# Kernel optimization log

Measured on AMD Instinct MI355X. Metric: run time of the kernel, lower is better.

## Reference

```python
import jax, jax.numpy as jnp
import numpy as np
jax.config.update('jax_enable_x64', True)

H = 16          # tree height -> n = 2**H
TP = 16         # parallel coordinate dims
F = 2
DIV = 2
K = F * H // DIV          # 16
N = 1 << H                # 65536
EMB = 1_000_000
T = 2048                  # rows in this block


def setup_inputs() -> dict:
    key = jax.random.key(0)
    k1, k2, k3 = jax.random.split(key, 3)
    # location table: signed ints in [1-n, n), as in torch.randint(1-n, n, ...)
    locations = jax.random.randint(k1, (EMB, TP), 1 - N, N, dtype=jnp.int64)
    pos_idx = jax.random.randint(k2, (T,), 0, EMB, dtype=jnp.int64)
    norm = jax.random.uniform(k3, (T, 1, 1), dtype=jnp.float32)
    return {"locations": locations, "pos_idx": pos_idx, "norm": norm}


def _generate_random_masks(key, sz):
    # masks[i] uniform in [0, 2**i) per level i  (note: & binds looser than -,
    # so torch code computes rand & (2**i - 1))
    upper = (jnp.int64(1) << jnp.arange(H, dtype=jnp.int64)) - 1  # (H,)
    rn = jax.random.randint(key, (H, sz, K, TP), 0, N, dtype=jnp.int64)
    masks = rn & upper[:, None, None, None]
    return jnp.transpose(masks, (1, 0, 2, 3))  # (sz, H, K, TP)


def _connection(key, ori_int):
    # ori_int: (T, TP) int64
    kmask, kperm = jax.random.split(key)
    flip_masks = (jnp.int64(1) << jnp.arange(H, dtype=jnp.int64))[None, :, None]  # (1,H,1)
    flipped = ori_int[:, None, :] ^ flip_masks                    # (T, H, TP)
    rmasks = _generate_random_masks(kmask, flipped.shape[0])      # (T, H, K, TP)
    result = (flipped[:, :, None, :] ^ rmasks).reshape(T, H * K, TP)
    loc = jnp.concatenate([result, ori_int[:, None, :], -result], axis=1)  # (T, 2HK+1, TP)
    perm = jax.random.permutation(kperm, loc.shape[1])
    return loc[:, perm, :]


def _distance(coord1, coord2, norm):
    # sign product: +1 if same sign (>=0 vs <0), else -1
    sg = (jnp.where(coord1 >= 0, 1.0, -1.0) * jnp.where(coord2 >= 0, 1.0, -1.0)).astype(jnp.float32)
    xor = jnp.abs(coord1) ^ jnp.abs(coord2)
    _, e = jnp.frexp((xor + 1).astype(jnp.float32))  # frexp exponent == bit length
    s = e.astype(jnp.float32) / H
    return sg * (1.0 - s) * norm


def reference(locations, pos_idx, norm):
    # gather this block's node locations (irregular gather from large table)
    ori = locations[pos_idx]                         # (T, TP)
    key = jax.random.key(42)
    loc = _connection(key, ori)                      # (T, 2HK+1, TP) candidate neighbors
    # distances from each candidate back to the original location
    return _distance(loc, ori[:, None, :], norm)     # (T, 2HK+1, TP) float32
```

## Files before the change

### kernel.cpp

```cpp
#include <hip/hip_runtime.h>
#include <stdint.h>


#define H_   16
#define TP_  16
#define K_   16
#define T_   2048
#define NC   513
#define ROWS 4
#define GRID (T_ / ROWS)

typedef float f32x4 __attribute__((ext_vector_type(4)));

struct TFPair { uint32_t a, b; };

__host__ __device__ constexpr uint32_t rotl32(uint32_t x, int r) {
  return (x << r) | (x >> (32 - r));
}

__host__ __device__ constexpr TFPair tf2x32(uint32_t k0, uint32_t k1,
                                            uint32_t x0, uint32_t x1) {
  uint32_t ks0 = k0, ks1 = k1, ks2 = k0 ^ k1 ^ 0x1BD11BDAu;
  x0 += ks0; x1 += ks1;
  x0 += x1; x1 = rotl32(x1, 13); x1 ^= x0;
  x0 += x1; x1 = rotl32(x1, 15); x1 ^= x0;
  x0 += x1; x1 = rotl32(x1, 26); x1 ^= x0;
  x0 += x1; x1 = rotl32(x1,  6); x1 ^= x0;
  x0 += ks1; x1 += ks2 + 1u;
  x0 += x1; x1 = rotl32(x1, 17); x1 ^= x0;
  x0 += x1; x1 = rotl32(x1, 29); x1 ^= x0;
  x0 += x1; x1 = rotl32(x1, 16); x1 ^= x0;
  x0 += x1; x1 = rotl32(x1, 24); x1 ^= x0;
  x0 += ks2; x1 += ks0 + 2u;
  x0 += x1; x1 = rotl32(x1, 13); x1 ^= x0;
  x0 += x1; x1 = rotl32(x1, 15); x1 ^= x0;
  x0 += x1; x1 = rotl32(x1, 26); x1 ^= x0;
  x0 += x1; x1 = rotl32(x1,  6); x1 ^= x0;
  x0 += ks0; x1 += ks1 + 3u;
  x0 += x1; x1 = rotl32(x1, 17); x1 ^= x0;
  x0 += x1; x1 = rotl32(x1, 29); x1 ^= x0;
  x0 += x1; x1 = rotl32(x1, 16); x1 ^= x0;
  x0 += x1; x1 = rotl32(x1, 24); x1 ^= x0;
  x0 += ks1; x1 += ks2 + 4u;
  x0 += x1; x1 = rotl32(x1, 13); x1 ^= x0;
  x0 += x1; x1 = rotl32(x1, 15); x1 ^= x0;
  x0 += x1; x1 = rotl32(x1, 26); x1 ^= x0;
  x0 += x1; x1 = rotl32(x1,  6); x1 ^= x0;
  x0 += ks2; x1 += ks0 + 5u;
  return {x0, x1};
}

constexpr TFPair KM = tf2x32(0u, 42u, 0u, 0u);
constexpr TFPair KP = tf2x32(0u, 42u, 0u, 1u);
constexpr TFPair C2 = tf2x32(KM.a, KM.b, 0u, 1u);
constexpr uint32_t KLO0 = C2.a, KLO1 = C2.b;
constexpr TFPair SB = tf2x32(KP.a, KP.b, 0u, 1u);
constexpr uint32_t KSUB0 = SB.a, KSUB1 = SB.b;

struct Keys { uint32_t v[NC]; };
constexpr Keys make_keys() {
  Keys k{};
  for (int i = 0; i < NC; ++i) {
    TFPair r = tf2x32(KSUB0, KSUB1, 0u, (uint32_t)i);
    k.v[i] = r.a ^ r.b;
  }
  return k;
}
constexpr Keys KEYS = make_keys();

#define PART_SZ 33
struct Part { int v[PART_SZ]; };
constexpr Part make_part(int lo) {
  Part p{};
  for (int m = lo; m < lo + PART_SZ && m < NC; ++m) {
    uint32_t km = KEYS.v[m];
    int rank = 0;
    for (int j = 0; j < NC; ++j) {
      uint32_t kj = KEYS.v[j];
      if (kj < km || (kj == km && j < m)) ++rank;
    }
    p.v[m - lo] = rank;
  }
  return p;
}
constexpr Part PT0  = make_part(0),   PT1  = make_part(33),
               PT2  = make_part(66),  PT3  = make_part(99),
               PT4  = make_part(132), PT5  = make_part(165),
               PT6  = make_part(198), PT7  = make_part(231),
               PT8  = make_part(264), PT9  = make_part(297),
               PT10 = make_part(330), PT11 = make_part(363),
               PT12 = make_part(396), PT13 = make_part(429),
               PT14 = make_part(462), PT15 = make_part(495);

struct IPerm { int v[NC]; };
constexpr IPerm merge_parts() {
  IPerm r{};
  const Part* ps[16] = {&PT0, &PT1, &PT2,  &PT3,  &PT4,  &PT5,  &PT6,  &PT7,
                        &PT8, &PT9, &PT10, &PT11, &PT12, &PT13, &PT14, &PT15};
  for (int c = 0; c < 16; ++c)
    for (int i = 0; i < PART_SZ; ++i) {
      int m = c * PART_SZ + i;
      if (m < NC) r.v[m] = ps[c]->v[i];
    }
  return r;
}
constexpr IPerm IPERM = merge_parts();
constexpr int C_ORI = IPERM.v[256];

struct CTab { uint32_t v[256]; };
constexpr CTab make_ctab() {
  CTab c{};
  for (int j = 0; j < 256; ++j)
    c.v[j] = (uint32_t)IPERM.v[j] | ((uint32_t)IPERM.v[j + 257] << 16);
  return c;
}
constexpr CTab CTAB = make_ctab();
__device__ __constant__ CTab d_ctab = CTAB;

__global__ __launch_bounds__(256, 4) void dist_kernel(
    const int* __restrict__ locations, const int* __restrict__ pos_idx,
    const float* __restrict__ norm, float* __restrict__ out) {
  __shared__ __align__(16) float buf[NC * TP_];

  const int tid = (int)threadIdx.x;
  const int tp  = tid & 15;
  const int jl  = tid >> 4;
  const int t0  = (int)blockIdx.x * ROWS;

  uint32_t ct[16];
#pragma unroll
  for (int i = 0; i < 16; ++i) ct[i] = d_ctab.v[(jl << 4) + i];

  const uint32_t flip_h = 1u << jl;
  const uint32_t mask_h = flip_h - 1u;
  const f32x4* __restrict__ b4 = (const f32x4*)buf;

  int   ori_c = locations[pos_idx[t0] * TP_ + tp];
  float nm_c  = norm[t0];

#pragma unroll 1
  for (int row = 0; row < ROWS; ++row) {
    const int t = t0 + row;

    int ori_n = 0; float nm_n = 0.0f;
    if (row + 1 < ROWS) {
      ori_n = locations[pos_idx[t + 1] * TP_ + tp];
      nm_n  = norm[t + 1];
    }

    const int   ori  = ori_c;
    const float nm   = nm_c;
    const float nm16 = nm * 0.0625f;
    const uint32_t ao   = (uint32_t)(ori < 0 ? -ori : ori);
    const uint32_t base = (uint32_t)(((jl * T_ + t) * K_) * TP_ + tp);

    if (tid < 16) buf[C_ORI * TP_ + tid] = 0.9375f * nm;

#pragma unroll
    for (int jj = 0; jj < 16; ++jj) {
      const TFPair r = tf2x32(KLO0, KLO1, 0u, base + (uint32_t)(jj * TP_));
      const uint32_t fm = flip_h ^ (r.b & mask_h);
      const int v = ori ^ (int)fm;

      const uint32_t sgbit = ((uint32_t)(v ^ ori)) & 0x80000000u;
      const uint32_t av = (uint32_t)(v < 0 ? -v : v);
      const uint32_t x  = (av ^ ao) + 1u;
      const int e = 32 - __clz((int)x);
      const float f  = nm - (float)e * nm16;
      const float d1 = __uint_as_float(__float_as_uint(f) ^ sgbit);
      const float d2 = (v == 0) ? d1
                     : __uint_as_float(__float_as_uint(d1) ^ 0x80000000u);

      const uint32_t pr = ct[jj];
      buf[(pr & 0xffffu) * TP_ + tp] = d1;
      buf[(pr >> 16)     * TP_ + tp] = d2;
    }

    __builtin_amdgcn_sched_barrier(0);
    asm volatile("s_waitcnt lgkmcnt(0)" ::: "memory");
    __builtin_amdgcn_s_barrier();
    __builtin_amdgcn_sched_barrier(0);

    f32x4* __restrict__ o4 = (f32x4*)(out + (size_t)t * (NC * TP_));
#pragma unroll
    for (int it = 0; it < 8; ++it)
      __builtin_nontemporal_store(b4[(it << 8) + tid], o4 + (it << 8) + tid);
    if (tid < 4)
      __builtin_nontemporal_store(b4[2048 + tid], o4 + 2048 + tid);

    __builtin_amdgcn_sched_barrier(0);
    asm volatile("" ::: "memory");
    __builtin_amdgcn_s_barrier();
    __builtin_amdgcn_sched_barrier(0);

    ori_c = ori_n; nm_c = nm_n;
  }
}

extern "C" void kernel_launch(void* const* d_in, const int* in_sizes, int n_in,
                              void* d_out, int out_size, void* d_ws, size_t ws_size,
                              hipStream_t stream) {
  const int*   locations = (const int*)d_in[0];
  const int*   pos_idx   = (const int*)d_in[1];
  const float* norm      = (const float*)d_in[2];
  float* out = (float*)d_out;

  hipLaunchKernelGGL(dist_kernel, dim3(GRID), dim3(256), 0, stream,
                     locations, pos_idx, norm, out);
}
```

Before: 118.0 us.

## Stage row output in registers and interleave global stores with next row compute

Each row's shared-memory tile is now read into eight register vectors after the barrier. Those vectors are written to global memory interleaved with the Threefry/distance computation of the following row, so store issue overlaps with ALU work instead of sitting in a separate phase. The first row is peeled off as a prologue and the last row's stores are flushed in an epilogue. The launch bounds drop from 4 to 2 blocks per CU to make room for the 32 extra staging registers, which may reduce occupancy-based latency hiding.

```diff
diff --git a/kernel.cpp b/kernel.cpp
--- a/kernel.cpp
+++ b/kernel.cpp
@@ -117,7 +117,51 @@
 constexpr CTab CTAB = make_ctab();
 __device__ __constant__ CTab d_ctab = CTAB;
 
-__global__ __launch_bounds__(256, 4) void dist_kernel(
+__device__ __forceinline__ void sbar_lgkm() {
+  __builtin_amdgcn_sched_barrier(0);
+  asm volatile("s_waitcnt lgkmcnt(0)" ::: "memory");
+  __builtin_amdgcn_s_barrier();
+  __builtin_amdgcn_sched_barrier(0);
+}
+
+template <bool DO_ST>
+__device__ __forceinline__ void compute_row(
+    int ori, float nm, uint32_t base, uint32_t flip_h, uint32_t mask_h,
+    const uint32_t* __restrict__ ct, float* __restrict__ buf,
+    int tid, int tp, const f32x4* __restrict__ stg, f32x4* __restrict__ o4p) {
+  const float nm16 = nm * 0.0625f;
+  const uint32_t ao = (uint32_t)(ori < 0 ? -ori : ori);
+
+  if (tid < 16) buf[C_ORI * TP_ + tid] = 0.9375f * nm;
+
+#pragma unroll
+  for (int jj = 0; jj < 16; ++jj) {
+    const TFPair r = tf2x32(KLO0, KLO1, 0u, base + (uint32_t)(jj * TP_));
+    const uint32_t fm = flip_h ^ (r.b & mask_h);
+    const int v = ori ^ (int)fm;
+
+    const uint32_t sgbit = ((uint32_t)(v ^ ori)) & 0x80000000u;
+    const uint32_t av = (uint32_t)(v < 0 ? -v : v);
+    const uint32_t x  = (av ^ ao) + 1u;
+    const int e = 32 - __clz((int)x);
+    const float f  = nm - (float)e * nm16;
+    const float d1 = __uint_as_float(__float_as_uint(f) ^ sgbit);
+    const float d2 = (v == 0) ? d1
+                   : __uint_as_float(__float_as_uint(d1) ^ 0x80000000u);
+
+    const uint32_t pr = ct[jj];
+    buf[(pr & 0xffffu) * TP_ + tp] = d1;
+    buf[(pr >> 16)     * TP_ + tp] = d2;
+
+    if (DO_ST && (jj & 1)) {
+      const int s = jj >> 1;
+      __builtin_nontemporal_store(stg[s], o4p + (s << 8) + tid);
+      __builtin_amdgcn_sched_barrier(0);
+    }
+  }
+}
+
+__global__ __launch_bounds__(256, 2) void dist_kernel(
     const int* __restrict__ locations, const int* __restrict__ pos_idx,
     const float* __restrict__ norm, float* __restrict__ out) {
   __shared__ __align__(16) float buf[NC * TP_];
@@ -135,65 +179,60 @@
   const uint32_t mask_h = flip_h - 1u;
   const f32x4* __restrict__ b4 = (const f32x4*)buf;
 
+  f32x4 stg[8];
+
   int   ori_c = locations[pos_idx[t0] * TP_ + tp];
   float nm_c  = norm[t0];
+  int   ori_n = locations[pos_idx[t0 + 1] * TP_ + tp];
+  float nm_n  = norm[t0 + 1];
+
+  {
+    const uint32_t base = (uint32_t)(((jl * T_ + t0) * K_) * TP_ + tp);
+    compute_row<false>(ori_c, nm_c, base, flip_h, mask_h, ct, buf, tid, tp,
+                       nullptr, nullptr);
+    sbar_lgkm();
+#pragma unroll
+    for (int s = 0; s < 8; ++s) stg[s] = b4[(s << 8) + tid];
+    if (tid < 4) {
+      f32x4 tl = b4[2048 + tid];
+      __builtin_nontemporal_store(
+          tl, (f32x4*)(out + (size_t)t0 * (NC * TP_)) + 2048 + tid);
+    }
+    sbar_lgkm();
+    ori_c = ori_n; nm_c = nm_n;
+  }
 
 #pragma unroll 1
-  for (int row = 0; row < ROWS; ++row) {
+  for (int row = 1; row < ROWS; ++row) {
     const int t = t0 + row;
-
-    int ori_n = 0; float nm_n = 0.0f;
     if (row + 1 < ROWS) {
       ori_n = locations[pos_idx[t + 1] * TP_ + tp];
       nm_n  = norm[t + 1];
     }
 
-    const int   ori  = ori_c;
-    const float nm   = nm_c;
-    const float nm16 = nm * 0.0625f;
-    const uint32_t ao   = (uint32_t)(ori < 0 ? -ori : ori);
+    f32x4* __restrict__ o4_prev = (f32x4*)(out + (size_t)(t - 1) * (NC * TP_));
     const uint32_t base = (uint32_t)(((jl * T_ + t) * K_) * TP_ + tp);
-
-    if (tid < 16) buf[C_ORI * TP_ + tid] = 0.9375f * nm;
-
-#pragma unroll
-    for (int jj = 0; jj < 16; ++jj) {
-      const TFPair r = tf2x32(KLO0, KLO1, 0u, base + (uint32_t)(jj * TP_));
-      const uint32_t fm = flip_h ^ (r.b & mask_h);
-      const int v = ori ^ (int)fm;
-
-      const uint32_t sgbit = ((uint32_t)(v ^ ori)) & 0x80000000u;
-      const uint32_t av = (uint32_t)(v < 0 ? -v : v);
-      const uint32_t x  = (av ^ ao) + 1u;
-      const int e = 32 - __clz((int)x);
-      const float f  = nm - (float)e * nm16;
-      const float d1 = __uint_as_float(__float_as_uint(f) ^ sgbit);
-      const float d2 = (v == 0) ? d1
-                     : __uint_as_float(__float_as_uint(d1) ^ 0x80000000u);
-
-      const uint32_t pr = ct[jj];
-      buf[(pr & 0xffffu) * TP_ + tp] = d1;
-      buf[(pr >> 16)     * TP_ + tp] = d2;
-    }
-
-    __builtin_amdgcn_sched_barrier(0);
-    asm volatile("s_waitcnt lgkmcnt(0)" ::: "memory");
-    __builtin_amdgcn_s_barrier();
-    __builtin_amdgcn_sched_barrier(0);
-
-    f32x4* __restrict__ o4 = (f32x4*)(out + (size_t)t * (NC * TP_));
-#pragma unroll
-    for (int it = 0; it < 8; ++it)
-      __builtin_nontemporal_store(b4[(it << 8) + tid], o4 + (it << 8) + tid);
-    if (tid < 4)
-      __builtin_nontemporal_store(b4[2048 + tid], o4 + 2048 + tid);
-
-    __builtin_amdgcn_sched_barrier(0);
-    asm volatile("" ::: "memory");
-    __builtin_amdgcn_s_barrier();
-    __builtin_amdgcn_sched_barrier(0);
-
+    compute_row<true>(ori_c, nm_c, base, flip_h, mask_h, ct, buf, tid, tp,
+                      stg, o4_prev);
+
+    sbar_lgkm();
+#pragma unroll
+    for (int s = 0; s < 8; ++s) stg[s] = b4[(s << 8) + tid];
+    if (tid < 4) {
+      f32x4 tl = b4[2048 + tid];
+      __builtin_nontemporal_store(
+          tl, (f32x4*)(out + (size_t)t * (NC * TP_)) + 2048 + tid);
+    }
+    sbar_lgkm();
     ori_c = ori_n; nm_c = nm_n;
+  }
+
+  {
+    f32x4* __restrict__ o4 =
+        (f32x4*)(out + (size_t)(t0 + ROWS - 1) * (NC * TP_));
+#pragma unroll
+    for (int s = 0; s < 8; ++s)
+      __builtin_nontemporal_store(stg[s], o4 + (s << 8) + tid);
   }
 }
 
```

Measured after the change: 117.8 us. No clear change (-0.1%).
